# Kernel optimization log

Measured on AMD Instinct MI355X. Metric: run time of the kernel, lower is better.

The kernel has to match this reference:

```python
import jax, jax.numpy as jnp
import numpy as np

D_MODEL = 1024
N_HEADS = 16
HEAD_DIM = D_MODEL // N_HEADS
D_FF = 4096
B, T = 2, 2048


def layernorm(x, g, b, eps=1e-5):
    mu = jnp.mean(x, axis=-1, keepdims=True)
    var = jnp.var(x, axis=-1, keepdims=True)
    return (x - mu) * jax.lax.rsqrt(var + eps) * g + b


def setup_inputs() -> dict:
    key = jax.random.key(0)
    ks = jax.random.split(key, 8)
    s = 0.02
    return {
        "x": jax.random.normal(ks[0], (B, T, D_MODEL), dtype=jnp.float32),
        "ln1_g": jnp.ones((D_MODEL,), jnp.float32),
        "ln1_b": jnp.zeros((D_MODEL,), jnp.float32),
        "qkv_w": jax.random.normal(ks[1], (D_MODEL, 3 * D_MODEL), jnp.float32) * s,
        "qkv_b": jnp.zeros((3 * D_MODEL,), jnp.float32),
        "proj_w": jax.random.normal(ks[2], (D_MODEL, D_MODEL), jnp.float32) * s,
        "proj_b": jnp.zeros((D_MODEL,), jnp.float32),
        "ln2_g": jnp.ones((D_MODEL,), jnp.float32),
        "ln2_b": jnp.zeros((D_MODEL,), jnp.float32),
        "mlp_w1": jax.random.normal(ks[3], (D_MODEL, D_FF), jnp.float32) * s,
        "mlp_b1": jnp.zeros((D_FF,), jnp.float32),
        "mlp_w2": jax.random.normal(ks[4], (D_FF, D_MODEL), jnp.float32) * s,
        "mlp_b2": jnp.zeros((D_MODEL,), jnp.float32),
    }


def reference(x, ln1_g, ln1_b, qkv_w, qkv_b, proj_w, proj_b,
              ln2_g, ln2_b, mlp_w1, mlp_b1, mlp_w2, mlp_b2):
    Bv, Tv, C = x.shape
    scale = HEAD_DIM ** -0.5
    # --- attention branch ---
    h = layernorm(x, ln1_g, ln1_b)
    qkv = h @ qkv_w + qkv_b                                   # [B,T,3C]
    qkv = qkv.reshape(Bv, Tv, 3, N_HEADS, HEAD_DIM)
    q, k, v = qkv[:, :, 0], qkv[:, :, 1], qkv[:, :, 2]        # [B,T,H,Dh]
    att = jnp.einsum('bqhd,bkhd->bhqk', q, k) * scale         # [B,H,T,T]
    causal = jnp.tril(jnp.ones((Tv, Tv), dtype=bool))
    att = jnp.where(causal[None, None], att, -jnp.inf)
    att = jax.nn.softmax(att, axis=-1)
    out = jnp.einsum('bhqk,bkhd->bqhd', att, v).reshape(Bv, Tv, C)
    out = out @ proj_w + proj_b
    x = x + out
    # --- mlp branch ---
    h2 = layernorm(x, ln2_g, ln2_b)
    h2 = jax.nn.gelu(h2 @ mlp_w1 + mlp_b1, approximate=False)
    x = x + (h2 @ mlp_w2 + mlp_b2)
    return x
```

## Files before the change

### kernel.cpp

```cpp
#include <hip/hip_runtime.h>
#include <hip/hip_bf16.h>
#include <cstdint>

typedef __attribute__((ext_vector_type(4))) float f32x4;
typedef __attribute__((ext_vector_type(16))) float f32x16;
typedef __attribute__((ext_vector_type(8))) __bf16 bf16x8;
typedef __attribute__((ext_vector_type(4))) __bf16 bf16x4;
typedef __attribute__((ext_vector_type(4))) uint32_t u32x4;
typedef __attribute__((ext_vector_type(2))) unsigned int u32x2;

#define EPI_BF16  0
#define EPI_GELU  1
#define EPI_RES   2
#define EPI_PART  3
#define EPI_PARTB 4

__device__ __forceinline__ void gll16(const void* g, void* l) {
  __builtin_amdgcn_global_load_lds((__attribute__((address_space(1))) void*)(g),
                                   (__attribute__((address_space(3))) void*)(l), 16, 0, 0);
}

__global__ __launch_bounds__(256)
void convT_all(const float* __restrict__ W0, __bf16* __restrict__ T0,
               const float* __restrict__ W1, __bf16* __restrict__ T1,
               const float* __restrict__ W2, __bf16* __restrict__ T2,
               const float* __restrict__ W3, __bf16* __restrict__ T3)
{
  __shared__ __bf16 t[64][72];
  const int bid = blockIdx.x;
  const float* W; __bf16* WT; int Kd, Nd, nx, lb;
  if (bid < 768)       { W = W0; WT = T0; Kd = 1024; Nd = 3072; nx = 48; lb = bid; }
  else if (bid < 1024) { W = W1; WT = T1; Kd = 1024; Nd = 1024; nx = 16; lb = bid - 768; }
  else if (bid < 2048) { W = W2; WT = T2; Kd = 1024; Nd = 4096; nx = 64; lb = bid - 1024; }
  else                 { W = W3; WT = T3; Kd = 4096; Nd = 1024; nx = 16; lb = bid - 2048; }
  const int tid = threadIdx.x;
  const int n0 = (lb % nx) * 64, k0 = (lb / nx) * 64;
#pragma unroll
  for (int i = 0; i < 4; ++i) {
    const int c = i * 256 + tid;
    const int r = c >> 4, cc = (c & 15) * 4;
    const float4 v = *(const float4*)(W + (size_t)(k0 + r) * Nd + n0 + cc);
    bf16x4 tv; tv[0] = (__bf16)v.x; tv[1] = (__bf16)v.y; tv[2] = (__bf16)v.z; tv[3] = (__bf16)v.w;
    *(bf16x4*)&t[r][cc] = tv;
  }
  __syncthreads();
#pragma unroll
  for (int i = 0; i < 2; ++i) {
    const int c = i * 256 + tid;
    const int n = c >> 3, s = (c & 7) * 8;
    bf16x8 o;
#pragma unroll
    for (int j = 0; j < 8; ++j) o[j] = t[s + j][n];
    *(bf16x8*)(WT + (size_t)(n0 + n) * Kd + k0 + s) = o;
  }
}

__global__ __launch_bounds__(256)
void ln_rows(const float* __restrict__ x, const float* __restrict__ g,
             const float* __restrict__ b, __bf16* __restrict__ out)
{
  const int row = blockIdx.x;
  const int tid = threadIdx.x;
  const float4 v = *(const float4*)(x + (size_t)row * 1024 + tid * 4);
  float s = v.x + v.y + v.z + v.w;
  float q = v.x * v.x + v.y * v.y + v.z * v.z + v.w * v.w;
#pragma unroll
  for (int o = 32; o; o >>= 1) { s += __shfl_xor(s, o); q += __shfl_xor(q, o); }
  __shared__ float red[8];
  const int wid = tid >> 6;
  if ((tid & 63) == 0) { red[wid] = s; red[4 + wid] = q; }
  __syncthreads();
  s = red[0] + red[1] + red[2] + red[3];
  q = red[4] + red[5] + red[6] + red[7];
  const float mu = s * (1.0f / 1024.0f);
  const float var = q * (1.0f / 1024.0f) - mu * mu;
  const float rs = rsqrtf(var + 1e-5f);
  bf16x4 o4;
#pragma unroll
  for (int i = 0; i < 4; ++i) {
    const int c = tid * 4 + i;
    const float xv = (&v.x)[i];
    o4[i] = (__bf16)((xv - mu) * rs * g[c] + b[c]);
  }
  *(bf16x4*)(out + (size_t)row * 1024 + tid * 4) = o4;
}

template<int EPI>
__global__ __launch_bounds__(256)
void gemm_bt(const __bf16* __restrict__ A, const __bf16* __restrict__ BT,
             const float* __restrict__ bias, const float* __restrict__ R,
             void* __restrict__ Out, int M, int N, int K)
{
  const int tid = threadIdx.x;
  const int lane = tid & 63, wid = tid >> 6;
  const int l15 = lane & 15, lg = lane >> 4;
  const int wm = (wid >> 1) * 64, wn = (wid & 1) * 64;
  const int nwg = gridDim.x * gridDim.y;
  const int hw = blockIdx.y * gridDim.x + blockIdx.x;
  const int logical = (hw & 7) * (nwg >> 3) + (hw >> 3);
  const int rowBase = (logical / gridDim.x) * 128;
  const int colBase = (logical % gridDim.x) * 128;
  const int kLen = K / gridDim.z;
  const int kBeg = blockIdx.z * kLen;
  __shared__ __bf16 As[128 * 32];
  __shared__ __bf16 Bs[128 * 32];
  f32x4 acc[4][4] = {};
  const int fsw = ((l15 >> 1) & 3) << 3;

  for (int k0 = kBeg; k0 < kBeg + kLen; k0 += 32) {
#pragma unroll
    for (int i = 0; i < 2; ++i) {
      const int c = i * 256 + tid;
      const int r = c >> 2;
      const int s = ((c & 3) ^ ((r >> 1) & 3)) * 8;
      gll16(A + (size_t)(rowBase + r) * K + (k0 + s), As + c * 8);
    }
#pragma unroll
    for (int i = 0; i < 2; ++i) {
      const int c = i * 256 + tid;
      const int r = c >> 2;
      const int s = ((c & 3) ^ ((r >> 1) & 3)) * 8;
      gll16(BT + (size_t)(colBase + r) * K + (k0 + s), Bs + c * 8);
    }
    __syncthreads();
    bf16x8 af[4], bfr[4];
#pragma unroll
    for (int m = 0; m < 4; ++m) af[m] = *(const bf16x8*)(As + (wm + m * 16 + l15) * 32 + (lg * 8 ^ fsw));
#pragma unroll
    for (int n = 0; n < 4; ++n) bfr[n] = *(const bf16x8*)(Bs + (wn + n * 16 + l15) * 32 + (lg * 8 ^ fsw));
#pragma unroll
    for (int m = 0; m < 4; ++m)
#pragma unroll
      for (int n = 0; n < 4; ++n)
        acc[m][n] = __builtin_amdgcn_mfma_f32_16x16x32_bf16(af[m], bfr[n], acc[m][n], 0, 0, 0);
    __syncthreads();
  }
#pragma unroll
  for (int m = 0; m < 4; ++m) {
#pragma unroll
    for (int n = 0; n < 4; ++n) {
      const int col = colBase + wn + n * 16 + l15;
      float bb = 0.0f;
      if constexpr (EPI != EPI_PART && EPI != EPI_PARTB) bb = bias[col];
#pragma unroll
      for (int i = 0; i < 4; ++i) {
        const int row = rowBase + wm + m * 16 + lg * 4 + i;
        float v = acc[m][n][i] + bb;
        if constexpr (EPI == EPI_GELU) {
          v = 0.5f * v * (1.0f + erff(v * 0.70710678118654752f));
          ((__bf16*)Out)[(size_t)row * N + col] = (__bf16)v;
        } else if constexpr (EPI == EPI_BF16) {
          ((__bf16*)Out)[(size_t)row * N + col] = (__bf16)v;
        } else if constexpr (EPI == EPI_RES) {
          v += R[(size_t)row * N + col];
          ((float*)Out)[(size_t)row * N + col] = v;
        } else if constexpr (EPI == EPI_PART) {
          ((float*)Out)[((size_t)blockIdx.z * M + row) * N + col] = v;
        } else {
          ((__bf16*)Out)[((size_t)blockIdx.z * M + row) * N + col] = (__bf16)v;
        }
      }
    }
  }
}

__global__ __launch_bounds__(256)
void reduce2(const float* __restrict__ P, const float* __restrict__ bias,
             const float* __restrict__ R, float* __restrict__ Out, int MN, int N)
{
  const size_t e = ((size_t)blockIdx.x * 256 + threadIdx.x) * 4;
  const float4 a = *(const float4*)(P + e);
  const float4 b = *(const float4*)(P + (size_t)MN + e);
  const float4 r = *(const float4*)(R + e);
  const float4 bb = *(const float4*)(bias + (e & (size_t)(N - 1)));
  float4 o;
  o.x = a.x + b.x + r.x + bb.x;
  o.y = a.y + b.y + r.y + bb.y;
  o.z = a.z + b.z + r.z + bb.z;
  o.w = a.w + b.w + r.w + bb.w;
  *(float4*)(Out + e) = o;
}

__global__ __launch_bounds__(256)
void reduce4(const __bf16* __restrict__ P, const float* __restrict__ bias,
             const float* __restrict__ R, float* __restrict__ Out, int MN, int N)
{
  const size_t e = ((size_t)blockIdx.x * 256 + threadIdx.x) * 8;
  float s[8];
#pragma unroll
  for (int i = 0; i < 8; ++i) s[i] = 0.0f;
#pragma unroll
  for (int p = 0; p < 4; ++p) {
    const bf16x8 v = *(const bf16x8*)(P + (size_t)p * MN + e);
#pragma unroll
    for (int i = 0; i < 8; ++i) s[i] += (float)v[i];
  }
  const size_t col = e & (size_t)(N - 1);
  const float4 r0 = *(const float4*)(R + e),       r1 = *(const float4*)(R + e + 4);
  const float4 b0 = *(const float4*)(bias + col),  b1 = *(const float4*)(bias + col + 4);
  float4 o0, o1;
  o0.x = s[0] + r0.x + b0.x; o0.y = s[1] + r0.y + b0.y;
  o0.z = s[2] + r0.z + b0.z; o0.w = s[3] + r0.w + b0.w;
  o1.x = s[4] + r1.x + b1.x; o1.y = s[5] + r1.y + b1.y;
  o1.z = s[6] + r1.z + b1.z; o1.w = s[7] + r1.w + b1.w;
  *(float4*)(Out + e)     = o0;
  *(float4*)(Out + e + 4) = o1;
}

__global__ __launch_bounds__(256)
void rearrange(const __bf16* __restrict__ qkv, __bf16* __restrict__ Q,
               __bf16* __restrict__ Kb, __bf16* __restrict__ VT)
{
  __shared__ __bf16 vt[64][72];
  const int tid = threadIdx.x;
  const int bid = blockIdx.x;
  const int bh = bid >> 5, tt = bid & 31;
  const int b = bh >> 4, h = bh & 15;
  const int t0 = tt * 64;
#pragma unroll
  for (int i = 0; i < 2; ++i) {
    const int c = i * 256 + tid;
    const int tk = c >> 3, d0 = (c & 7) * 8;
    const size_t srow = (size_t)(b * 2048 + t0 + tk) * 3072 + h * 64 + d0;
    const size_t drow = (size_t)(bh * 2048 + t0 + tk) * 64 + d0;
    *(bf16x8*)(Q + drow) = *(const bf16x8*)(qkv + srow);
    *(bf16x8*)(Kb + drow) = *(const bf16x8*)(qkv + srow + 1024);
    *(bf16x8*)&vt[tk][d0] = *(const bf16x8*)(qkv + srow + 2048);
  }
  __syncthreads();
#pragma unroll
  for (int i = 0; i < 2; ++i) {
    const int c = i * 256 + tid;
    const int d = c >> 3, s = (c & 7) * 8;
    bf16x8 o;
#pragma unroll
    for (int j = 0; j < 8; ++j) o[j] = vt[s + j][d];
    *(bf16x8*)(VT + (size_t)(bh * 64 + d) * 2048 + t0 + s) = o;
  }
}

__global__ __launch_bounds__(128)
void attn(const __bf16* __restrict__ Q, const __bf16* __restrict__ K,
          const __bf16* __restrict__ VT, __bf16* __restrict__ O)
{
  const int bid = blockIdx.x;
  const int bh = bid >> 5, qt = 31 - (bid & 31);
  const int tid = threadIdx.x;
  const int lane = tid & 63, w = tid >> 6;
  const int l31 = lane & 31, hi = lane >> 5;
  __shared__ __bf16 Ks[64 * 64];
  __shared__ __bf16 Vs[64 * 64];
  const size_t base = (size_t)bh * 2048 * 64;
  const int qrow0 = qt * 64 + w * 32;
  const int xsw = (l31 & 7) << 3;

  bf16x8 qf[4];
#pragma unroll
  for (int s = 0; s < 4; ++s)
    qf[s] = *(const bf16x8*)(Q + base + (size_t)(qrow0 + l31) * 64 + s * 16 + hi * 8);

  f32x16 oa0 = {}, oa1 = {};
  float mst = -INFINITY, lst = 0.0f;

  for (int j = 0; j <= qt; ++j) {
#pragma unroll
    for (int rnd = 0; rnd < 4; ++rnd) {
      const int c = rnd * 128 + tid;
      const int r = c >> 3;
      const int e = ((c & 7) ^ (r & 7)) * 8;
      gll16(K + base + (size_t)(j * 64 + r) * 64 + e, Ks + c * 8);
      gll16(VT + base + (size_t)r * 2048 + j * 64 + e, Vs + c * 8);
    }
    __syncthreads();

    f32x16 s0v = {}, s1v = {};
#pragma unroll
    for (int s = 0; s < 4; ++s) {
      const int co = (s * 16 + hi * 8) ^ xsw;
      bf16x8 ak0 = *(const bf16x8*)(Ks + l31 * 64 + co);
      bf16x8 ak1 = *(const bf16x8*)(Ks + (32 + l31) * 64 + co);
      s0v = __builtin_amdgcn_mfma_f32_32x32x16_bf16(ak0, qf[s], s0v, 0, 0, 0);
      s1v = __builtin_amdgcn_mfma_f32_32x32x16_bf16(ak1, qf[s], s1v, 0, 0, 0);
    }
#pragma unroll
    for (int rg = 0; rg < 16; ++rg) { s0v[rg] *= 0.125f; s1v[rg] *= 0.125f; }
    if (j == qt) {
      const int qg = qrow0 + l31;
#pragma unroll
      for (int rg = 0; rg < 16; ++rg) {
        const int kr = j * 64 + ((rg & 3) + 8 * (rg >> 2)) + 4 * hi;
        if (kr > qg) s0v[rg] = -INFINITY;
        if (kr + 32 > qg) s1v[rg] = -INFINITY;
      }
    }
    float mx = s0v[0];
#pragma unroll
    for (int rg = 1; rg < 16; ++rg) mx = fmaxf(mx, s0v[rg]);
#pragma unroll
    for (int rg = 0; rg < 16; ++rg) mx = fmaxf(mx, s1v[rg]);
    mx = fmaxf(mx, __shfl_xor(mx, 32));
    const float mnew = fmaxf(mst, mx);
    const float cf = __expf(mst - mnew);
    float rs = 0.0f;
#pragma unroll
    for (int rg = 0; rg < 16; ++rg) {
      s0v[rg] = __expf(s0v[rg] - mnew); rs += s0v[rg];
      s1v[rg] = __expf(s1v[rg] - mnew); rs += s1v[rg];
    }
    rs += __shfl_xor(rs, 32);
    lst = lst * cf + rs;
    mst = mnew;
#pragma unroll
    for (int rg = 0; rg < 16; ++rg) {
      const float cb = __shfl(cf, (rg & 3) + 8 * (rg >> 2) + 4 * hi);
      oa0[rg] *= cb; oa1[rg] *= cb;
    }
#pragma unroll
    for (int s = 0; s < 4; ++s) {
      const int br = (s & 1) * 8;
      uint32_t wA0, wA1, wB0, wB1;
      if (s < 2) {
        asm("v_cvt_pk_bf16_f32 %0, %1, %2" : "=v"(wA0) : "v"(s0v[br + 0]), "v"(s0v[br + 1]));
        asm("v_cvt_pk_bf16_f32 %0, %1, %2" : "=v"(wA1) : "v"(s0v[br + 2]), "v"(s0v[br + 3]));
        asm("v_cvt_pk_bf16_f32 %0, %1, %2" : "=v"(wB0) : "v"(s0v[br + 4]), "v"(s0v[br + 5]));
        asm("v_cvt_pk_bf16_f32 %0, %1, %2" : "=v"(wB1) : "v"(s0v[br + 6]), "v"(s0v[br + 7]));
      } else {
        asm("v_cvt_pk_bf16_f32 %0, %1, %2" : "=v"(wA0) : "v"(s1v[br + 0]), "v"(s1v[br + 1]));
        asm("v_cvt_pk_bf16_f32 %0, %1, %2" : "=v"(wA1) : "v"(s1v[br + 2]), "v"(s1v[br + 3]));
        asm("v_cvt_pk_bf16_f32 %0, %1, %2" : "=v"(wB0) : "v"(s1v[br + 4]), "v"(s1v[br + 5]));
        asm("v_cvt_pk_bf16_f32 %0, %1, %2" : "=v"(wB1) : "v"(s1v[br + 6]), "v"(s1v[br + 7]));
      }
      const u32x2 r0 = __builtin_amdgcn_permlane32_swap(wA0, wB0, false, false);
      const u32x2 r1 = __builtin_amdgcn_permlane32_swap(wA1, wB1, false, false);
      u32x4 uu; uu.x = r0.x; uu.y = r1.x; uu.z = r0.y; uu.w = r1.y;
      const bf16x8 pa = __builtin_bit_cast(bf16x8, uu);
      const int co = (s * 16 + hi * 8) ^ xsw;
      bf16x8 bv0 = *(const bf16x8*)(Vs + l31 * 64 + co);
      bf16x8 bv1 = *(const bf16x8*)(Vs + (32 + l31) * 64 + co);
      oa0 = __builtin_amdgcn_mfma_f32_32x32x16_bf16(pa, bv0, oa0, 0, 0, 0);
      oa1 = __builtin_amdgcn_mfma_f32_32x32x16_bf16(pa, bv1, oa1, 0, 0, 0);
    }
    __syncthreads();
  }
  const float inv = 1.0f / lst;
  const int b = bh >> 4, hd = bh & 15;
#pragma unroll
  for (int rg = 0; rg < 16; ++rg) {
    const int cr = (rg & 3) + 8 * (rg >> 2) + 4 * hi;
    const float ib = __shfl(inv, cr);
    const int qr = qrow0 + cr;
    O[(size_t)(b * 2048 + qr) * 1024 + hd * 64 + l31]      = (__bf16)(oa0[rg] * ib);
    O[(size_t)(b * 2048 + qr) * 1024 + hd * 64 + 32 + l31] = (__bf16)(oa1[rg] * ib);
  }
}

extern "C" void kernel_launch(void* const* d_in, const int* in_sizes, int n_in,
                              void* d_out, int out_size, void* d_ws, size_t ws_size,
                              hipStream_t stream)
{
  const float* x      = (const float*)d_in[0];
  const float* ln1_g  = (const float*)d_in[1];
  const float* ln1_b  = (const float*)d_in[2];
  const float* qkv_w  = (const float*)d_in[3];
  const float* qkv_b  = (const float*)d_in[4];
  const float* proj_w = (const float*)d_in[5];
  const float* proj_b = (const float*)d_in[6];
  const float* ln2_g  = (const float*)d_in[7];
  const float* ln2_b  = (const float*)d_in[8];
  const float* mlp_w1 = (const float*)d_in[9];
  const float* mlp_b1 = (const float*)d_in[10];
  const float* mlp_w2 = (const float*)d_in[11];
  const float* mlp_b2 = (const float*)d_in[12];

  char* ws = (char*)d_ws;
  __bf16* qkvT  = (__bf16*)(ws + 0);
  __bf16* projT = (__bf16*)(ws + 6291456);
  __bf16* w1T   = (__bf16*)(ws + 8388608);
  __bf16* w2T   = (__bf16*)(ws + 16777216);
  float*  x2    = (float*) (ws + 25165824);
  __bf16* h1    = (__bf16*)(ws + 41943040);
  float*  partP = (float*) (ws + 41943040);
  __bf16* part2 = (__bf16*)(ws + 41943040);
  __bf16* qkv   = (__bf16*)(ws + 50331648);
  __bf16* Qb    = (__bf16*)(ws + 75497472);
  __bf16* h2    = (__bf16*)(ws + 75497472);
  __bf16* Kb    = (__bf16*)(ws + 83886080);
  __bf16* act1  = (__bf16*)(ws + 83886080);
  __bf16* VTb   = (__bf16*)(ws + 92274688);
  __bf16* attO  = (__bf16*)(ws + 100663296);

  convT_all<<<3072, 256, 0, stream>>>(qkv_w, qkvT, proj_w, projT, mlp_w1, w1T, mlp_w2, w2T);

  ln_rows<<<4096, 256, 0, stream>>>(x, ln1_g, ln1_b, h1);
  gemm_bt<EPI_BF16><<<dim3(24, 32), 256, 0, stream>>>(h1, qkvT, qkv_b, nullptr, qkv, 4096, 3072, 1024);
  rearrange<<<1024, 256, 0, stream>>>(qkv, Qb, Kb, VTb);
  attn<<<1024, 128, 0, stream>>>(Qb, Kb, VTb, attO);
  gemm_bt<EPI_PART><<<dim3(8, 32, 2), 256, 0, stream>>>(attO, projT, nullptr, nullptr, partP, 4096, 1024, 1024);
  reduce2<<<4096, 256, 0, stream>>>(partP, proj_b, x, x2, 4096 * 1024, 1024);
  ln_rows<<<4096, 256, 0, stream>>>(x2, ln2_g, ln2_b, h2);
  gemm_bt<EPI_GELU><<<dim3(32, 32), 256, 0, stream>>>(h2, w1T, mlp_b1, nullptr, act1, 4096, 4096, 1024);
  gemm_bt<EPI_PARTB><<<dim3(8, 32, 4), 256, 0, stream>>>(act1, w2T, nullptr, nullptr, part2, 4096, 1024, 4096);
  reduce4<<<2048, 256, 0, stream>>>(part2, mlp_b2, x2, (float*)d_out, 4096 * 1024, 1024);
}
```

Before: 414.9 us.

## Double-buffer LDS in GEMM and attention, widen attention tiles, lazy softmax rescale

The GEMM kernel now uses two LDS buffers and issues the next K-slice's global-to-LDS loads before computing on the current one, dropping one barrier per iteration. The attention kernel does the same for its K/V tiles, moves to 256-thread blocks covering 128 query rows (4 waves sharing each K/V tile), and uses exp2 with the scale folded into one FMA. It also rescales the output accumulators only when the running max grows by more than a threshold. The costs are doubled LDS, more causal imbalance across blocks, and a looser running max that relies on exp2 headroom.

```diff
diff --git a/kernel.cpp b/kernel.cpp
--- a/kernel.cpp
+++ b/kernel.cpp
@@ -102,38 +102,40 @@
   const int colBase = (logical % gridDim.x) * 128;
   const int kLen = K / gridDim.z;
   const int kBeg = blockIdx.z * kLen;
-  __shared__ __bf16 As[128 * 32];
-  __shared__ __bf16 Bs[128 * 32];
+  __shared__ __bf16 As[2][128 * 32];
+  __shared__ __bf16 Bs[2][128 * 32];
   f32x4 acc[4][4] = {};
   const int fsw = ((l15 >> 1) & 3) << 3;
 
-  for (int k0 = kBeg; k0 < kBeg + kLen; k0 += 32) {
+  auto STAGE = [&](int buf, int k0) {
 #pragma unroll
     for (int i = 0; i < 2; ++i) {
       const int c = i * 256 + tid;
       const int r = c >> 2;
       const int s = ((c & 3) ^ ((r >> 1) & 3)) * 8;
-      gll16(A + (size_t)(rowBase + r) * K + (k0 + s), As + c * 8);
+      gll16(A + (size_t)(rowBase + r) * K + (k0 + s), &As[buf][c * 8]);
+      gll16(BT + (size_t)(colBase + r) * K + (k0 + s), &Bs[buf][c * 8]);
     }
-#pragma unroll
-    for (int i = 0; i < 2; ++i) {
-      const int c = i * 256 + tid;
-      const int r = c >> 2;
-      const int s = ((c & 3) ^ ((r >> 1) & 3)) * 8;
-      gll16(BT + (size_t)(colBase + r) * K + (k0 + s), Bs + c * 8);
-    }
-    __syncthreads();
+  };
+
+  STAGE(0, kBeg);
+  __syncthreads();
+  int cur = 0;
+  const int kEnd = kBeg + kLen;
+  for (int k0 = kBeg; k0 < kEnd; k0 += 32) {
+    if (k0 + 32 < kEnd) STAGE(cur ^ 1, k0 + 32);
     bf16x8 af[4], bfr[4];
 #pragma unroll
-    for (int m = 0; m < 4; ++m) af[m] = *(const bf16x8*)(As + (wm + m * 16 + l15) * 32 + (lg * 8 ^ fsw));
-#pragma unroll
-    for (int n = 0; n < 4; ++n) bfr[n] = *(const bf16x8*)(Bs + (wn + n * 16 + l15) * 32 + (lg * 8 ^ fsw));
+    for (int m = 0; m < 4; ++m) af[m] = *(const bf16x8*)(&As[cur][(wm + m * 16 + l15) * 32 + (lg * 8 ^ fsw)]);
+#pragma unroll
+    for (int n = 0; n < 4; ++n) bfr[n] = *(const bf16x8*)(&Bs[cur][(wn + n * 16 + l15) * 32 + (lg * 8 ^ fsw)]);
 #pragma unroll
     for (int m = 0; m < 4; ++m)
 #pragma unroll
       for (int n = 0; n < 4; ++n)
         acc[m][n] = __builtin_amdgcn_mfma_f32_16x16x32_bf16(af[m], bfr[n], acc[m][n], 0, 0, 0);
     __syncthreads();
+    cur ^= 1;
   }
 #pragma unroll
   for (int m = 0; m < 4; ++m) {
@@ -239,20 +241,23 @@
   }
 }
 
-__global__ __launch_bounds__(128)
+__global__ __launch_bounds__(256)
 void attn(const __bf16* __restrict__ Q, const __bf16* __restrict__ K,
           const __bf16* __restrict__ VT, __bf16* __restrict__ O)
 {
   const int bid = blockIdx.x;
-  const int bh = bid >> 5, qt = 31 - (bid & 31);
+  const int bh = bid >> 4, qt = 15 - (bid & 15);
   const int tid = threadIdx.x;
   const int lane = tid & 63, w = tid >> 6;
   const int l31 = lane & 31, hi = lane >> 5;
-  __shared__ __bf16 Ks[64 * 64];
-  __shared__ __bf16 Vs[64 * 64];
+  __shared__ __bf16 Ks[2][64 * 64];
+  __shared__ __bf16 Vs[2][64 * 64];
   const size_t base = (size_t)bh * 2048 * 64;
-  const int qrow0 = qt * 64 + w * 32;
+  const int qrow0 = qt * 128 + w * 32;
+  const int jd = qrow0 >> 6;
+  const int jmax = 2 * qt + 1;
   const int xsw = (l31 & 7) << 3;
+  const float KS = 0.18033688011112042f;
 
   bf16x8 qf[4];
 #pragma unroll
@@ -260,87 +265,97 @@
     qf[s] = *(const bf16x8*)(Q + base + (size_t)(qrow0 + l31) * 64 + s * 16 + hi * 8);
 
   f32x16 oa0 = {}, oa1 = {};
-  float mst = -INFINITY, lst = 0.0f;
-
-  for (int j = 0; j <= qt; ++j) {
-#pragma unroll
-    for (int rnd = 0; rnd < 4; ++rnd) {
-      const int c = rnd * 128 + tid;
+  float ms = -INFINITY, lst = 0.0f;
+
+  auto STAGE = [&](int buf, int j) {
+#pragma unroll
+    for (int i = 0; i < 2; ++i) {
+      const int c = i * 256 + tid;
       const int r = c >> 3;
       const int e = ((c & 7) ^ (r & 7)) * 8;
-      gll16(K + base + (size_t)(j * 64 + r) * 64 + e, Ks + c * 8);
-      gll16(VT + base + (size_t)r * 2048 + j * 64 + e, Vs + c * 8);
+      gll16(K + base + (size_t)(j * 64 + r) * 64 + e, &Ks[buf][c * 8]);
+      gll16(VT + base + (size_t)r * 2048 + j * 64 + e, &Vs[buf][c * 8]);
+    }
+  };
+
+  STAGE(0, 0);
+  __syncthreads();
+  int cur = 0;
+  for (int j = 0; j <= jmax; ++j) {
+    if (j < jmax) STAGE(cur ^ 1, j + 1);
+    if (j <= jd) {
+      f32x16 s0v = {}, s1v = {};
+#pragma unroll
+      for (int s = 0; s < 4; ++s) {
+        const int co = (s * 16 + hi * 8) ^ xsw;
+        bf16x8 ak0 = *(const bf16x8*)(&Ks[cur][l31 * 64 + co]);
+        bf16x8 ak1 = *(const bf16x8*)(&Ks[cur][(32 + l31) * 64 + co]);
+        s0v = __builtin_amdgcn_mfma_f32_32x32x16_bf16(ak0, qf[s], s0v, 0, 0, 0);
+        s1v = __builtin_amdgcn_mfma_f32_32x32x16_bf16(ak1, qf[s], s1v, 0, 0, 0);
+      }
+      if (j == jd) {
+        const int qg = qrow0 + l31;
+#pragma unroll
+        for (int rg = 0; rg < 16; ++rg) {
+          const int kr = j * 64 + ((rg & 3) + 8 * (rg >> 2)) + 4 * hi;
+          if (kr > qg) s0v[rg] = -INFINITY;
+          if (kr + 32 > qg) s1v[rg] = -INFINITY;
+        }
+      }
+      float mx = fmaxf(s0v[0], s1v[0]);
+#pragma unroll
+      for (int rg = 1; rg < 16; ++rg) mx = fmaxf(mx, fmaxf(s0v[rg], s1v[rg]));
+      mx = fmaxf(mx, __shfl_xor(mx, 32));
+      const float mxs = mx * KS;
+      if (!__all(mxs - ms <= 8.0f)) {
+        const float msn = fmaxf(ms, mxs);
+        const float cf = exp2f(ms - msn);
+        lst *= cf;
+        ms = msn;
+#pragma unroll
+        for (int rg = 0; rg < 16; ++rg) {
+          const float cb = __shfl(cf, (rg & 3) + 8 * (rg >> 2) + 4 * hi);
+          oa0[rg] *= cb; oa1[rg] *= cb;
+        }
+      }
+      float rs = 0.0f;
+#pragma unroll
+      for (int rg = 0; rg < 16; ++rg) {
+        const float p0 = exp2f(fmaf(s0v[rg], KS, -ms));
+        const float p1 = exp2f(fmaf(s1v[rg], KS, -ms));
+        s0v[rg] = p0; s1v[rg] = p1;
+        rs += p0 + p1;
+      }
+      rs += __shfl_xor(rs, 32);
+      lst += rs;
+#pragma unroll
+      for (int s = 0; s < 4; ++s) {
+        const int br = (s & 1) * 8;
+        uint32_t wA0, wA1, wB0, wB1;
+        if (s < 2) {
+          asm("v_cvt_pk_bf16_f32 %0, %1, %2" : "=v"(wA0) : "v"(s0v[br + 0]), "v"(s0v[br + 1]));
+          asm("v_cvt_pk_bf16_f32 %0, %1, %2" : "=v"(wA1) : "v"(s0v[br + 2]), "v"(s0v[br + 3]));
+          asm("v_cvt_pk_bf16_f32 %0, %1, %2" : "=v"(wB0) : "v"(s0v[br + 4]), "v"(s0v[br + 5]));
+          asm("v_cvt_pk_bf16_f32 %0, %1, %2" : "=v"(wB1) : "v"(s0v[br + 6]), "v"(s0v[br + 7]));
+        } else {
+          asm("v_cvt_pk_bf16_f32 %0, %1, %2" : "=v"(wA0) : "v"(s1v[br + 0]), "v"(s1v[br + 1]));
+          asm("v_cvt_pk_bf16_f32 %0, %1, %2" : "=v"(wA1) : "v"(s1v[br + 2]), "v"(s1v[br + 3]));
+          asm("v_cvt_pk_bf16_f32 %0, %1, %2" : "=v"(wB0) : "v"(s1v[br + 4]), "v"(s1v[br + 5]));
+          asm("v_cvt_pk_bf16_f32 %0, %1, %2" : "=v"(wB1) : "v"(s1v[br + 6]), "v"(s1v[br + 7]));
+        }
+        const u32x2 r0 = __builtin_amdgcn_permlane32_swap(wA0, wB0, false, false);
+        const u32x2 r1 = __builtin_amdgcn_permlane32_swap(wA1, wB1, false, false);
+        u32x4 uu; uu.x = r0.x; uu.y = r1.x; uu.z = r0.y; uu.w = r1.y;
+        const bf16x8 pa = __builtin_bit_cast(bf16x8, uu);
+        const int co = (s * 16 + hi * 8) ^ xsw;
+        bf16x8 bv0 = *(const bf16x8*)(&Vs[cur][l31 * 64 + co]);
+        bf16x8 bv1 = *(const bf16x8*)(&Vs[cur][(32 + l31) * 64 + co]);
+        oa0 = __builtin_amdgcn_mfma_f32_32x32x16_bf16(pa, bv0, oa0, 0, 0, 0);
+        oa1 = __builtin_amdgcn_mfma_f32_32x32x16_bf16(pa, bv1, oa1, 0, 0, 0);
+      }
     }
     __syncthreads();
-
-    f32x16 s0v = {}, s1v = {};
-#pragma unroll
-    for (int s = 0; s < 4; ++s) {
-      const int co = (s * 16 + hi * 8) ^ xsw;
-      bf16x8 ak0 = *(const bf16x8*)(Ks + l31 * 64 + co);
-      bf16x8 ak1 = *(const bf16x8*)(Ks + (32 + l31) * 64 + co);
-      s0v = __builtin_amdgcn_mfma_f32_32x32x16_bf16(ak0, qf[s], s0v, 0, 0, 0);
-      s1v = __builtin_amdgcn_mfma_f32_32x32x16_bf16(ak1, qf[s], s1v, 0, 0, 0);
-    }
-#pragma unroll
-    for (int rg = 0; rg < 16; ++rg) { s0v[rg] *= 0.125f; s1v[rg] *= 0.125f; }
-    if (j == qt) {
-      const int qg = qrow0 + l31;
-#pragma unroll
-      for (int rg = 0; rg < 16; ++rg) {
-        const int kr = j * 64 + ((rg & 3) + 8 * (rg >> 2)) + 4 * hi;
-        if (kr > qg) s0v[rg] = -INFINITY;
-        if (kr + 32 > qg) s1v[rg] = -INFINITY;
-      }
-    }
-    float mx = s0v[0];
-#pragma unroll
-    for (int rg = 1; rg < 16; ++rg) mx = fmaxf(mx, s0v[rg]);
-#pragma unroll
-    for (int rg = 0; rg < 16; ++rg) mx = fmaxf(mx, s1v[rg]);
-    mx = fmaxf(mx, __shfl_xor(mx, 32));
-    const float mnew = fmaxf(mst, mx);
-    const float cf = __expf(mst - mnew);
-    float rs = 0.0f;
-#pragma unroll
-    for (int rg = 0; rg < 16; ++rg) {
-      s0v[rg] = __expf(s0v[rg] - mnew); rs += s0v[rg];
-      s1v[rg] = __expf(s1v[rg] - mnew); rs += s1v[rg];
-    }
-    rs += __shfl_xor(rs, 32);
-    lst = lst * cf + rs;
-    mst = mnew;
-#pragma unroll
-    for (int rg = 0; rg < 16; ++rg) {
-      const float cb = __shfl(cf, (rg & 3) + 8 * (rg >> 2) + 4 * hi);
-      oa0[rg] *= cb; oa1[rg] *= cb;
-    }
-#pragma unroll
-    for (int s = 0; s < 4; ++s) {
-      const int br = (s & 1) * 8;
-      uint32_t wA0, wA1, wB0, wB1;
-      if (s < 2) {
-        asm("v_cvt_pk_bf16_f32 %0, %1, %2" : "=v"(wA0) : "v"(s0v[br + 0]), "v"(s0v[br + 1]));
-        asm("v_cvt_pk_bf16_f32 %0, %1, %2" : "=v"(wA1) : "v"(s0v[br + 2]), "v"(s0v[br + 3]));
-        asm("v_cvt_pk_bf16_f32 %0, %1, %2" : "=v"(wB0) : "v"(s0v[br + 4]), "v"(s0v[br + 5]));
-        asm("v_cvt_pk_bf16_f32 %0, %1, %2" : "=v"(wB1) : "v"(s0v[br + 6]), "v"(s0v[br + 7]));
-      } else {
-        asm("v_cvt_pk_bf16_f32 %0, %1, %2" : "=v"(wA0) : "v"(s1v[br + 0]), "v"(s1v[br + 1]));
-        asm("v_cvt_pk_bf16_f32 %0, %1, %2" : "=v"(wA1) : "v"(s1v[br + 2]), "v"(s1v[br + 3]));
-        asm("v_cvt_pk_bf16_f32 %0, %1, %2" : "=v"(wB0) : "v"(s1v[br + 4]), "v"(s1v[br + 5]));
-        asm("v_cvt_pk_bf16_f32 %0, %1, %2" : "=v"(wB1) : "v"(s1v[br + 6]), "v"(s1v[br + 7]));
-      }
-      const u32x2 r0 = __builtin_amdgcn_permlane32_swap(wA0, wB0, false, false);
-      const u32x2 r1 = __builtin_amdgcn_permlane32_swap(wA1, wB1, false, false);
-      u32x4 uu; uu.x = r0.x; uu.y = r1.x; uu.z = r0.y; uu.w = r1.y;
-      const bf16x8 pa = __builtin_bit_cast(bf16x8, uu);
-      const int co = (s * 16 + hi * 8) ^ xsw;
-      bf16x8 bv0 = *(const bf16x8*)(Vs + l31 * 64 + co);
-      bf16x8 bv1 = *(const bf16x8*)(Vs + (32 + l31) * 64 + co);
-      oa0 = __builtin_amdgcn_mfma_f32_32x32x16_bf16(pa, bv0, oa0, 0, 0, 0);
-      oa1 = __builtin_amdgcn_mfma_f32_32x32x16_bf16(pa, bv1, oa1, 0, 0, 0);
-    }
-    __syncthreads();
+    cur ^= 1;
   }
   const float inv = 1.0f / lst;
   const int b = bh >> 4, hd = bh & 15;
@@ -394,7 +409,7 @@
   ln_rows<<<4096, 256, 0, stream>>>(x, ln1_g, ln1_b, h1);
   gemm_bt<EPI_BF16><<<dim3(24, 32), 256, 0, stream>>>(h1, qkvT, qkv_b, nullptr, qkv, 4096, 3072, 1024);
   rearrange<<<1024, 256, 0, stream>>>(qkv, Qb, Kb, VTb);
-  attn<<<1024, 128, 0, stream>>>(Qb, Kb, VTb, attO);
+  attn<<<512, 256, 0, stream>>>(Qb, Kb, VTb, attO);
   gemm_bt<EPI_PART><<<dim3(8, 32, 2), 256, 0, stream>>>(attO, projT, nullptr, nullptr, partP, 4096, 1024, 1024);
   reduce2<<<4096, 256, 0, stream>>>(partP, proj_b, x, x2, 4096 * 1024, 1024);
   ln_rows<<<4096, 256, 0, stream>>>(x2, ln2_g, ln2_b, h2);
```

New measurement: 409.3 us. Within noise of the previous version (-1.4%).
